# Optimization experiments

Hardware: AMD Instinct MI355X
Metric: run time of the kernel (lower is better)

Reference implementation:

```python
import jax, jax.numpy as jnp
import numpy as np

TEMP = 1.0
BETA = 0.5
ALPHA = 0.5
GAMMA = 0.5


def _pairwise_sqdist(x, y):
    # squared euclidean distances [N, M]; clamp tiny negatives from cancellation
    xx = jnp.sum(x * x, axis=-1)
    yy = jnp.sum(y * y, axis=-1)
    d = xx[:, None] + yy[None, :] - 2.0 * (x @ y.T)
    return jnp.maximum(d, 0.0)


def setup_inputs() -> dict:
    key = jax.random.key(0)
    features = jax.random.normal(key, (16384, 128), dtype=jnp.float32)
    return {"features": features}


def reference(features):
    B = features.shape[0] // 2
    a = features[:B]
    b = features[B:]
    t2 = TEMP * TEMP

    # Positive term: only the diagonal of sim_ab is used, so compute it directly.
    # sim = 1 / ((temperature * cdist)^2 + 1) = 1 / (t^2 * sqdist + 1)
    pos_sq = jnp.sum((a - b) ** 2, axis=-1)              # [B]
    pos_sim = 1.0 / (t2 * pos_sq + 1.0)
    positive_loss = jnp.mean((pos_sim - 10.0) ** 2 - 2.0 * ALPHA * pos_sim)

    eye = jnp.eye(B, dtype=bool)

    def _neg(x):
        sim = 1.0 / (t2 * _pairwise_sqdist(x, x) + 1.0)   # [B, B]
        sim = jnp.where(eye, 0.0, sim)                     # zero the diagonal
        neg_loss = jnp.mean(jnp.sum(jnp.exp(BETA * sim) * sim, axis=-1))
        return neg_loss, jnp.sum(sim)

    nl_a, s_a = _neg(a)
    nl_b, s_b = _neg(b)

    negative_loss = nl_a + nl_b
    regularization = GAMMA * (s_a + s_b)
    return positive_loss + negative_loss + regularization
```

## Files before the change

kernel.cpp:

```cpp
#include <hip/hip_runtime.h>
#include <hip/hip_bf16.h>


typedef __attribute__((ext_vector_type(8))) short short8;
typedef __attribute__((ext_vector_type(4))) float float4v;

#define NROWS 16384
#define BHALF 8192
#define D 128
#define NT 64
#define NPAIRS 2080
#define NACC 64
#define NPART 256

__device__ __forceinline__ unsigned short f2bf(float x) {
    unsigned int u = __float_as_uint(x);
    u += 0x7fffu + ((u >> 16) & 1u);
    return (unsigned short)(u >> 16);
}

__global__ __launch_bounds__(512)
void prep_pos_kernel(const float* __restrict__ f,
                     unsigned short* __restrict__ xbf,
                     float* __restrict__ xx,
                     float* __restrict__ part,
                     float* __restrict__ negacc) {
    __shared__ float red[8];
    const int wave = threadIdx.x >> 6, lane = threadIdx.x & 63;
    const int gw = blockIdx.x * 8 + wave;
    float posAcc = 0.0f;

    #pragma unroll
    for (int p = 0; p < 4; ++p) {
        const int i = gw + p * 2048;
        const float2 a = *reinterpret_cast<const float2*>(f + (size_t)i * D + lane * 2);
        const float2 b = *reinterpret_cast<const float2*>(f + (size_t)(i + BHALF) * D + lane * 2);
        ushort2 sa2, sb2;
        sa2.x = f2bf(a.x); sa2.y = f2bf(a.y);
        sb2.x = f2bf(b.x); sb2.y = f2bf(b.y);
        *reinterpret_cast<ushort2*>(xbf + (size_t)i * D + lane * 2) = sa2;
        *reinterpret_cast<ushort2*>(xbf + (size_t)(i + BHALF) * D + lane * 2) = sb2;
        float sa = a.x * a.x + a.y * a.y;
        float sb = b.x * b.x + b.y * b.y;
        float dx = a.x - b.x, dy = a.y - b.y;
        float sp = dx * dx + dy * dy;
        #pragma unroll
        for (int off = 32; off; off >>= 1) {
            sa += __shfl_down(sa, off, 64);
            sb += __shfl_down(sb, off, 64);
            sp += __shfl_down(sp, off, 64);
        }
        if (lane == 0) {
            xx[i] = sa;
            xx[i + BHALF] = sb;
            float ps = 1.0f / (sp + 1.0f);
            posAcc += (ps - 10.0f) * (ps - 10.0f) - ps;
        }
    }
    if (lane == 0) red[wave] = posAcc;
    if (blockIdx.x == 0 && threadIdx.x < NACC) negacc[threadIdx.x] = 0.0f;
    __syncthreads();
    if (threadIdx.x == 0) {
        float s = 0.0f;
        #pragma unroll
        for (int w = 0; w < 8; ++w) s += red[w];
        part[blockIdx.x] = s;
    }
}

__global__ __launch_bounds__(512, 8)
void neg_kernel(const unsigned short* __restrict__ xbf,
                const float* __restrict__ xx,
                float* __restrict__ negacc) {
    __shared__ unsigned short lB[128 * 128];
    __shared__ float red[16];

    const int t = threadIdx.x;
    const int mat = blockIdx.y;
    const int moff = mat * BHALF;

    int rem = blockIdx.x, bi = 0;
    while (rem >= NT - bi) { rem -= NT - bi; ++bi; }
    const int tbi = bi, tbj = bi + rem;

    const int wave = t >> 6, lane = t & 63;
    const int wr = wave >> 1, wc = wave & 1;
    const int l15 = lane & 15, g = lane >> 4;

    {
        const char* gbase = (const char*)(xbf + (size_t)(moff + tbj * 128) * D);
        #pragma unroll
        for (int p = 0; p < 4; ++p) {
            const int c = p * 512 + t;
            const int row = c >> 4, col16 = c & 15;
            const int gb = row * 256 + ((col16 * 16) ^ ((row & 7) << 4));
            const unsigned ldsoff = (unsigned)(p * 512 + wave * 64) * 16;
            __builtin_amdgcn_global_load_lds(
                (const __attribute__((address_space(1))) unsigned int*)(gbase + gb),
                (__attribute__((address_space(3))) unsigned int*)((char*)lB + ldsoff),
                16, 0, 0);
        }
    }

    const unsigned short* Aubase =
        xbf + ((size_t)(moff + tbi * 128 + wr * 32 + l15) * D + g * 8);

    __syncthreads();

    float4v accv[2][4] = {};

    #pragma unroll
    for (int kk = 0; kk < 4; ++kk) {
        short8 a[2], b[4];
        #pragma unroll
        for (int mi = 0; mi < 2; ++mi)
            a[mi] = *reinterpret_cast<const short8*>(Aubase + mi * 16 * D + kk * 32);
        #pragma unroll
        for (int ni = 0; ni < 4; ++ni) {
            const int trow = wc * 64 + ni * 16 + l15;
            const int boff = (kk * 64 + g * 16) ^ ((trow & 7) << 4);
            b[ni] = *reinterpret_cast<short8*>(reinterpret_cast<char*>(lB) + trow * 256 + boff);
        }
        #pragma unroll
        for (int mi = 0; mi < 2; ++mi)
            #pragma unroll
            for (int ni = 0; ni < 4; ++ni)
                accv[mi][ni] = __builtin_amdgcn_mfma_f32_16x16x32_bf16(a[mi], b[ni], accv[mi][ni], 0, 0, 0);
    }

    const bool diag = (tbi == tbj);
    const int rbase = tbi * 128 + wr * 32;
    const int cbase = tbj * 128 + wc * 64;

    float xr1[8], xc[4];
    #pragma unroll
    for (int mi = 0; mi < 2; ++mi)
        #pragma unroll
        for (int r = 0; r < 4; ++r)
            xr1[mi * 4 + r] = xx[moff + rbase + mi * 16 + g * 4 + r] + 1.0f;
    #pragma unroll
    for (int ni = 0; ni < 4; ++ni)
        xc[ni] = xx[moff + cbase + ni * 16 + l15];

    float aS0 = 0.0f, aS1 = 0.0f, aN0 = 0.0f, aN1 = 0.0f;
    #pragma unroll
    for (int mi = 0; mi < 2; ++mi) {
        #pragma unroll
        for (int ni = 0; ni < 4; ++ni) {
            #pragma unroll
            for (int r = 0; r < 4; ++r) {
                const float dot = accv[mi][ni][r];
                float t1 = xr1[mi * 4 + r] + xc[ni];
                float m = fmaxf(fmaf(dot, -2.0f, t1), 1.0f);
                float s = __builtin_amdgcn_rcpf(m);
                if (diag) {
                    const int row = rbase + mi * 16 + g * 4 + r;
                    const int col = cbase + ni * 16 + l15;
                    if (row == col) s = 0.0f;
                }
                float p = fmaf(s, 0.02083333333f, 0.125f);
                p = fmaf(s, p, 0.5f);
                p = fmaf(s, p, 1.0f);
                if (r & 1) { aS1 += s; aN1 = fmaf(p, s, aN1); }
                else       { aS0 += s; aN0 = fmaf(p, s, aN0); }
            }
        }
    }
    float aS = aS0 + aS1, aN = aN0 + aN1;

    #pragma unroll
    for (int off = 32; off; off >>= 1) {
        aS += __shfl_down(aS, off, 64);
        aN += __shfl_down(aN, off, 64);
    }
    if (lane == 0) { red[wave * 2] = aS; red[wave * 2 + 1] = aN; }
    __syncthreads();
    if (t == 0) {
        float S = 0.0f, N = 0.0f;
        #pragma unroll
        for (int w = 0; w < 8; ++w) { S += red[w * 2]; N += red[w * 2 + 1]; }
        const float w = diag ? 1.0f : 2.0f;
        atomicAdd(&negacc[(blockIdx.x * 2 + blockIdx.y) & (NACC - 1)],
                  w * (N * (1.0f / (float)BHALF) + 0.5f * S));
    }
}

__global__ void finish_kernel(const float* __restrict__ negacc,
                              const float* __restrict__ part,
                              float* __restrict__ out) {
    const int lane = threadIdx.x & 63;
    float v = negacc[lane];
    float pp = part[lane] + part[lane + 64] + part[lane + 128] + part[lane + 192];
    v = fmaf(pp, 1.0f / (float)BHALF, v);
    #pragma unroll
    for (int off = 32; off; off >>= 1) v += __shfl_down(v, off, 64);
    if (lane == 0) out[0] = v;
}

extern "C" void kernel_launch(void* const* d_in, const int* in_sizes, int n_in,
                              void* d_out, int out_size, void* d_ws, size_t ws_size,
                              hipStream_t stream) {
    const float* f = (const float*)d_in[0];
    float* out = (float*)d_out;
    unsigned short* xbf = (unsigned short*)d_ws;
    float* xx = (float*)((char*)d_ws + (size_t)NROWS * D * sizeof(unsigned short));
    float* negacc = xx + NROWS;
    float* part = negacc + NACC;

    prep_pos_kernel<<<NPART, 512, 0, stream>>>(f, xbf, xx, part, negacc);
    neg_kernel<<<dim3(NPAIRS, 2), 512, 0, stream>>>(xbf, xx, negacc);
    finish_kernel<<<1, 64, 0, stream>>>(negacc, part, out);
}
```

Measured before the change: 122.1 us.

## Fold sum and exp terms into one polynomial, preload A fragments, relax occupancy

The per-element exp-weighted term and the plain sum are merged algebraically into a single cubic polynomial in s, with pre-scaled coefficients. This leaves one accumulator instead of two and halves the shuffle reduction and the LDS traffic. All A-operand fragments are loaded into registers before the barrier so the global loads overlap the LDS fill. The launch-bounds occupancy hint drops from 8 to 4 to allow more registers, and the prep kernel batches its global loads ahead of compute. The extra registers may lower occupancy.

```diff
diff --git a/kernel.cpp b/kernel.cpp
--- a/kernel.cpp
+++ b/kernel.cpp
@@ -12,6 +12,11 @@
 #define NPAIRS 2080
 #define NACC 64
 #define NPART 256
+
+#define C0 0.5001220703125f
+#define C1 6.103515625e-5f
+#define C2 1.52587890625e-5f
+#define C3 2.5431315104e-6f
 
 __device__ __forceinline__ unsigned short f2bf(float x) {
     unsigned int u = __float_as_uint(x);
@@ -30,19 +35,25 @@
     const int gw = blockIdx.x * 8 + wave;
     float posAcc = 0.0f;
 
+    float2 av[4], bv[4];
     #pragma unroll
     for (int p = 0; p < 4; ++p) {
         const int i = gw + p * 2048;
-        const float2 a = *reinterpret_cast<const float2*>(f + (size_t)i * D + lane * 2);
-        const float2 b = *reinterpret_cast<const float2*>(f + (size_t)(i + BHALF) * D + lane * 2);
+        av[p] = *reinterpret_cast<const float2*>(f + (size_t)i * D + lane * 2);
+        bv[p] = *reinterpret_cast<const float2*>(f + (size_t)(i + BHALF) * D + lane * 2);
+    }
+
+    #pragma unroll
+    for (int p = 0; p < 4; ++p) {
+        const int i = gw + p * 2048;
         ushort2 sa2, sb2;
-        sa2.x = f2bf(a.x); sa2.y = f2bf(a.y);
-        sb2.x = f2bf(b.x); sb2.y = f2bf(b.y);
+        sa2.x = f2bf(av[p].x); sa2.y = f2bf(av[p].y);
+        sb2.x = f2bf(bv[p].x); sb2.y = f2bf(bv[p].y);
         *reinterpret_cast<ushort2*>(xbf + (size_t)i * D + lane * 2) = sa2;
         *reinterpret_cast<ushort2*>(xbf + (size_t)(i + BHALF) * D + lane * 2) = sb2;
-        float sa = a.x * a.x + a.y * a.y;
-        float sb = b.x * b.x + b.y * b.y;
-        float dx = a.x - b.x, dy = a.y - b.y;
+        float sa = av[p].x * av[p].x + av[p].y * av[p].y;
+        float sb = bv[p].x * bv[p].x + bv[p].y * bv[p].y;
+        float dx = av[p].x - bv[p].x, dy = av[p].y - bv[p].y;
         float sp = dx * dx + dy * dy;
         #pragma unroll
         for (int off = 32; off; off >>= 1) {
@@ -68,12 +79,12 @@
     }
 }
 
-__global__ __launch_bounds__(512, 8)
+__global__ __launch_bounds__(512, 4)
 void neg_kernel(const unsigned short* __restrict__ xbf,
                 const float* __restrict__ xx,
                 float* __restrict__ negacc) {
     __shared__ unsigned short lB[128 * 128];
-    __shared__ float red[16];
+    __shared__ float red[8];
 
     const int t = threadIdx.x;
     const int mat = blockIdx.y;
@@ -102,8 +113,16 @@
         }
     }
 
-    const unsigned short* Aubase =
-        xbf + ((size_t)(moff + tbi * 128 + wr * 32 + l15) * D + g * 8);
+    short8 a[2][4];
+    {
+        const unsigned short* Au =
+            xbf + ((size_t)(moff + tbi * 128 + wr * 32 + l15) * D + g * 8);
+        #pragma unroll
+        for (int mi = 0; mi < 2; ++mi)
+            #pragma unroll
+            for (int kk = 0; kk < 4; ++kk)
+                a[mi][kk] = *reinterpret_cast<const short8*>(Au + mi * 16 * D + kk * 32);
+    }
 
     __syncthreads();
 
@@ -111,10 +130,7 @@
 
     #pragma unroll
     for (int kk = 0; kk < 4; ++kk) {
-        short8 a[2], b[4];
-        #pragma unroll
-        for (int mi = 0; mi < 2; ++mi)
-            a[mi] = *reinterpret_cast<const short8*>(Aubase + mi * 16 * D + kk * 32);
+        short8 b[4];
         #pragma unroll
         for (int ni = 0; ni < 4; ++ni) {
             const int trow = wc * 64 + ni * 16 + l15;
@@ -125,7 +141,7 @@
         for (int mi = 0; mi < 2; ++mi)
             #pragma unroll
             for (int ni = 0; ni < 4; ++ni)
-                accv[mi][ni] = __builtin_amdgcn_mfma_f32_16x16x32_bf16(a[mi], b[ni], accv[mi][ni], 0, 0, 0);
+                accv[mi][ni] = __builtin_amdgcn_mfma_f32_16x16x32_bf16(a[mi][kk], b[ni], accv[mi][ni], 0, 0, 0);
     }
 
     const bool diag = (tbi == tbj);
@@ -142,7 +158,7 @@
     for (int ni = 0; ni < 4; ++ni)
         xc[ni] = xx[moff + cbase + ni * 16 + l15];
 
-    float aS0 = 0.0f, aS1 = 0.0f, aN0 = 0.0f, aN1 = 0.0f;
+    float acc0 = 0.0f, acc1 = 0.0f;
     #pragma unroll
     for (int mi = 0; mi < 2; ++mi) {
         #pragma unroll
@@ -158,30 +174,26 @@
                     const int col = cbase + ni * 16 + l15;
                     if (row == col) s = 0.0f;
                 }
-                float p = fmaf(s, 0.02083333333f, 0.125f);
-                p = fmaf(s, p, 0.5f);
-                p = fmaf(s, p, 1.0f);
-                if (r & 1) { aS1 += s; aN1 = fmaf(p, s, aN1); }
-                else       { aS0 += s; aN0 = fmaf(p, s, aN0); }
+                float u = fmaf(s, C3, C2);
+                u = fmaf(s, u, C1);
+                u = fmaf(s, u, C0);
+                if (r & 1) acc1 = fmaf(s, u, acc1);
+                else       acc0 = fmaf(s, u, acc0);
             }
         }
     }
-    float aS = aS0 + aS1, aN = aN0 + aN1;
-
-    #pragma unroll
-    for (int off = 32; off; off >>= 1) {
-        aS += __shfl_down(aS, off, 64);
-        aN += __shfl_down(aN, off, 64);
-    }
-    if (lane == 0) { red[wave * 2] = aS; red[wave * 2 + 1] = aN; }
+    float acc = acc0 + acc1;
+
+    #pragma unroll
+    for (int off = 32; off; off >>= 1) acc += __shfl_down(acc, off, 64);
+    if (lane == 0) red[wave] = acc;
     __syncthreads();
     if (t == 0) {
-        float S = 0.0f, N = 0.0f;
-        #pragma unroll
-        for (int w = 0; w < 8; ++w) { S += red[w * 2]; N += red[w * 2 + 1]; }
+        float S = 0.0f;
+        #pragma unroll
+        for (int w = 0; w < 8; ++w) S += red[w];
         const float w = diag ? 1.0f : 2.0f;
-        atomicAdd(&negacc[(blockIdx.x * 2 + blockIdx.y) & (NACC - 1)],
-                  w * (N * (1.0f / (float)BHALF) + 0.5f * S));
+        atomicAdd(&negacc[(blockIdx.x * 2 + blockIdx.y) & (NACC - 1)], w * S);
     }
 }
 
```

Result: no change. 122.1 us (+0.0%).
